# Kernel tuning notes

Hardware: AMD Instinct MI355X
Metric: run time of the kernel (lower is better)

The kernel has to match this reference:

```python
import jax, jax.numpy as jnp
import numpy as np

B, L, C, N, TN = 1, 256, 128, 4, 4
CH = N * C  # 512, flattened hidden for routing projections
EPS = 1.1920929e-07  # torch.finfo(float32).eps (RMSNorm default eps)
LN_EPS = 1e-5
N_SINKHORN = 20  # training-mode iteration count


def sinkhorn_knopp(raw, n_iters):
    # raw: [..., n, n] real-valued logits -> doubly-stochastic matrix
    M = jnp.exp(raw)
    for _ in range(n_iters):
        M = M / jnp.sum(M, axis=-1, keepdims=True)  # row normalize
        M = M / jnp.sum(M, axis=-2, keepdims=True)  # col normalize
    return M


def setup_inputs() -> dict:
    key = jax.random.key(0)
    ks = jax.random.split(key, 8)
    s = 0.02
    eye = jnp.eye(N, dtype=jnp.float32)
    b_res = 2.0 * eye + (-2.0) * (1.0 - eye)
    return {
        "p": jax.random.normal(ks[0], (B, L, L, C), jnp.float32),
        "p_mask": jnp.ones((B, L, L), jnp.float32),
        "W_pre": jax.random.normal(ks[1], (N, CH), jnp.float32) * s,
        "W_post": jax.random.normal(ks[2], (N, CH), jnp.float32) * s,
        "W_res": jax.random.normal(ks[3], (N * N, CH), jnp.float32) * s,
        "b_pre": jnp.zeros((1, N), jnp.float32),
        "b_post": jnp.zeros((1, N), jnp.float32),
        "b_res": b_res,
        "alpha_pre": jnp.asarray(0.01, jnp.float32),
        "alpha_post": jnp.asarray(0.01, jnp.float32),
        "alpha_res": jnp.asarray(0.01, jnp.float32),
        "ln_g": jnp.ones((C,), jnp.float32),
        "ln_b": jnp.zeros((C,), jnp.float32),
        "W1": jax.random.normal(ks[4], (TN * C, C), jnp.float32) * s,
        "b1": jnp.zeros((TN * C,), jnp.float32),
        "W2": jax.random.normal(ks[5], (C, TN * C), jnp.float32) * s,
        "b2": jnp.zeros((C,), jnp.float32),
    }


def reference(p, p_mask, W_pre, W_post, W_res, b_pre, b_post, b_res,
              alpha_pre, alpha_post, alpha_res, ln_g, ln_b, W1, b1, W2, b2):
    # expand_input: [B,L,L,C] -> [B,L,L,n,C]
    x = jnp.broadcast_to(p[..., None, :], (B, L, L, N, C))
    # --- compute_mappings ---
    xf = x.reshape(B, L, L, CH)
    xn = xf * jax.lax.rsqrt(jnp.mean(xf * xf, axis=-1, keepdims=True) + EPS)
    H_pre_dyn = jnp.tanh(xn @ W_pre.T)                      # [B,L,L,n]
    H_post_dyn = jnp.tanh(xn @ W_post.T)                    # [B,L,L,n]
    H_res_dyn = jnp.tanh(xn @ W_res.T).reshape(B, L, L, N, N)
    H_pre = jax.nn.sigmoid(alpha_pre * H_pre_dyn + b_pre)   # [B,L,L,n]
    H_post = 2.0 * jax.nn.sigmoid(alpha_post * H_post_dyn + b_post)
    H_res = sinkhorn_knopp(alpha_res * H_res_dyn + b_res, N_SINKHORN)  # [B,L,L,n,n]
    # contract: H_pre [B,L,L,1,n] @ x [B,L,L,n,C] -> [B,L,L,C]
    p_c = jnp.einsum('blkn,blknc->blkc', H_pre, x)
    # --- PairTransition (LN -> Linear -> ReLU -> Linear, masked) ---
    mu = jnp.mean(p_c, axis=-1, keepdims=True)
    var = jnp.mean(jnp.square(p_c - mu), axis=-1, keepdims=True)
    m = (p_c - mu) * jax.lax.rsqrt(var + LN_EPS) * ln_g + ln_b
    h = jax.nn.relu(m @ W1.T + b1)                          # [B,L,L,TN*C]
    p_t = (h @ W2.T + b2) * p_mask[..., None]
    p_updated = p_c + p_t
    # expand back: H_post^T [B,L,L,n,1] * p_updated [B,L,L,1,C]
    p_expanded = H_post[..., :, None] * p_updated[..., None, :]
    # residual mixing: [B,L,L,n,n] @ [B,L,L,n,C]
    p_residual = jnp.einsum('blkmn,blknc->blkmc', H_res, x)
    return p_residual + p_expanded  # [B,L,L,n,C]
```

## Files before the change

### kernel.cpp

```cpp
#include <hip/hip_runtime.h>
#include <stdint.h>

#define LLTOT 65536
#define CDIM  128
#define TPIX  32

typedef float f32x4  __attribute__((ext_vector_type(4)));
typedef float f32x16 __attribute__((ext_vector_type(16)));
typedef short s16x8  __attribute__((ext_vector_type(8)));

#define MFMA16(a, b, c) __builtin_amdgcn_mfma_f32_16x16x32_bf16((a), (b), (c), 0, 0, 0)
#define MFMA32(a, b, c) __builtin_amdgcn_mfma_f32_32x32x16_bf16((a), (b), (c), 0, 0, 0)

__device__ __align__(16) unsigned short g_wefff[2 * 4 * 64 * 8];
__device__ __align__(16) unsigned short g_w1gf[32 * 4 * 64 * 8];
__device__ __align__(16) unsigned short g_w2f [4 * 32 * 64 * 8];
__device__ __align__(16) float  g_hA[512];
__device__ __align__(16) float  g_w1gs[512];

__device__ __forceinline__ unsigned short f2bf(float f) {
    union { float f; uint32_t u; } v; v.f = f;
    uint32_t u = v.u;
    return (unsigned short)((u + 0x7FFFu + ((u >> 16) & 1u)) >> 16);
}
__device__ __forceinline__ uint32_t pack2(float a, float b) {
    uint32_t r;
    asm("v_cvt_pk_bf16_f32 %0, %1, %2" : "=v"(r) : "v"(a), "v"(b));
    return r;
}
__device__ __forceinline__ float bf2f(uint32_t lo16) { return __uint_as_float(lo16 << 16); }

__device__ __forceinline__ float fast_tanh(float x) {
    float cx = fminf(fmaxf(x, -10.f), 10.f);
    float e = __expf(2.f * cx);
    return (e - 1.f) * __builtin_amdgcn_rcpf(e + 1.f);
}
__device__ __forceinline__ float fast_sig(float z) {
    return __builtin_amdgcn_rcpf(1.f + __expf(-z));
}

__global__ void prep_kernel(const float* __restrict__ Wpre, const float* __restrict__ Wpost,
                            const float* __restrict__ Wres, const float* __restrict__ W1,
                            const float* __restrict__ W2, const float* __restrict__ ln_g,
                            const float* __restrict__ ln_b, const float* __restrict__ b1) {
    int b = blockIdx.x, t = threadIdx.x;
    if (b == 264) {
        int j = t;
        float sg = 0.f, sb = 0.f;
        const float* row = W1 + j * 128;
        #pragma unroll 4
        for (int c = 0; c < 128; c += 4) {
            float4 wv = *(const float4*)(row + c);
            float4 gv = *(const float4*)(ln_g + c);
            float4 bv = *(const float4*)(ln_b + c);
            sg += wv.x*gv.x + wv.y*gv.y + wv.z*gv.z + wv.w*gv.w;
            sb += wv.x*bv.x + wv.y*bv.y + wv.z*bv.z + wv.w*bv.w;
        }
        g_hA[j]   = b1[j] + sb;
        g_w1gs[j] = sg;
        return;
    }
    int idx = b * 512 + t;
    if (idx < 4096) {
        int e = idx & 7, lane = (idx >> 3) & 63, kk = (idx >> 9) & 3, tile = idx >> 11;
        int o = tile * 16 + (lane & 15);
        int c = kk * 32 + (lane >> 4) * 8 + e;
        float v = 0.f;
        if (o < 4)        v = Wpre[o*512+c] + Wpre[o*512+128+c] + Wpre[o*512+256+c] + Wpre[o*512+384+c];
        else if (o < 8)   { int j = o - 4;  v = Wpost[j*512+c] + Wpost[j*512+128+c] + Wpost[j*512+256+c] + Wpost[j*512+384+c]; }
        else if (o < 24)  { int j = o - 8;  v = Wres[j*512+c] + Wres[j*512+128+c] + Wres[j*512+256+c] + Wres[j*512+384+c]; }
        g_wefff[idx] = f2bf(v);
    } else if (idx < 69632) {
        int d = idx - 4096;
        int e = d & 7, lane = (d >> 3) & 63, kk = (d >> 9) & 3, jt = d >> 11;
        int j = jt * 16 + (lane & 15);
        int c = kk * 32 + (lane >> 4) * 8 + e;
        g_w1gf[d] = f2bf(W1[j * 128 + c] * ln_g[c]);
    } else if (idx < 135168) {
        int d = idx - 69632;
        int e = d & 7, lane = (d >> 3) & 63, kk = (d >> 9) & 31, ct = (d >> 14) & 3;
        int c = ct * 32 + (lane & 31);
        int k = kk * 16 + (lane >> 5) * 8 + e;
        g_w2f[d] = f2bf(W2[c * 512 + k]);
    }
}

__global__ void __launch_bounds__(512, 2) fused_kernel(
    const float* __restrict__ p, const float* __restrict__ p_mask,
    const float* __restrict__ b_pre, const float* __restrict__ b_post, const float* __restrict__ b_res,
    const float* __restrict__ a_pre, const float* __restrict__ a_post, const float* __restrict__ a_res,
    const float* __restrict__ b2g, float* __restrict__ out)
{
    __shared__ __align__(16) unsigned short pf_lds[8 * 64 * 8];
    __shared__ __align__(16) unsigned short h32[32 * 64 * 8];
    __shared__ __align__(16) float red_s[4096];
    __shared__ __align__(16) float A_s[128], B_s[128];
    __shared__ __align__(16) float2 simi_s[32];

    const int t = threadIdx.x;
    const int w = t >> 6, l = t & 63, lr = l & 15, lk = l >> 4;
    const size_t base = (size_t)blockIdx.x * TPIX;

    float M0 = 0.f, M1 = 0.f, M2 = 0.f, M3 = 0.f, sp = 0.f, hpm = 0.f;
    int mrow = 0, pix = 0;

    if (w < 2) {
        const int g = lk, pixl = lr;
        const size_t gpix = base + w * 16 + pixl;
        float apre = a_pre[0], apost = a_post[0], ares = a_res[0];
        float msk = p_mask[gpix];
        float bp0 = b_pre[0], bp1 = b_pre[1], bp2 = b_pre[2], bp3 = b_pre[3];
        float bq0 = b_post[0], bq1 = b_post[1], bq2 = b_post[2], bq3 = b_post[3];
        mrow = (g + 2) & 3;
        float br0 = b_res[mrow*4+0], br1 = b_res[mrow*4+1], br2 = b_res[mrow*4+2], br3 = b_res[mrow*4+3];

        float s = 0.f, ss = 0.f;
        s16x8 pf[4];
        const float* prow = p + gpix * 128 + g * 8;
        #pragma unroll
        for (int kk = 0; kk < 4; ++kk) {
            float4 va = *(const float4*)(prow + kk * 32);
            float4 vb = *(const float4*)(prow + kk * 32 + 4);
            s  += va.x + va.y + va.z + va.w + vb.x + vb.y + vb.z + vb.w;
            ss += va.x*va.x + va.y*va.y + va.z*va.z + va.w*va.w
                + vb.x*vb.x + vb.y*vb.y + vb.z*vb.z + vb.w*vb.w;
            union { s16x8 v; uint32_t u[4]; } cc;
            cc.u[0] = pack2(va.x, va.y);
            cc.u[1] = pack2(va.z, va.w);
            cc.u[2] = pack2(vb.x, vb.y);
            cc.u[3] = pack2(vb.z, vb.w);
            pf[kk] = cc.v;
            *(s16x8*)(pf_lds + (size_t)(w * 4 + kk) * 512 + l * 8) = cc.v;
        }
        s  += __shfl_xor(s, 16);  ss += __shfl_xor(ss, 16);
        s  += __shfl_xor(s, 32);  ss += __shfl_xor(ss, 32);
        float mu = s * (1.f / 128.f), mq = ss * (1.f / 128.f);
        float rv  = rsqrtf(mq + 1.1920929e-07f);
        float var = mq - mu * mu;

        f32x4 y1 = {0.f, 0.f, 0.f, 0.f}, y2 = {0.f, 0.f, 0.f, 0.f};
        #pragma unroll
        for (int kk = 0; kk < 4; ++kk) {
            s16x8 a0 = *(const s16x8*)(g_wefff + ((size_t)(kk) * 64 + l) * 8);
            s16x8 a1 = *(const s16x8*)(g_wefff + ((size_t)(4 + kk) * 64 + l) * 8);
            y1 = MFMA16(a0, pf[kk], y1);
            y2 = MFMA16(a1, pf[kk], y2);
        }
        #pragma unroll
        for (int r = 0; r < 4; ++r) { y1[r] *= rv; y2[r] *= rv; }

        float sp_loc = fast_sig(apre * fast_tanh(y1[0]) + bp0)
                     + fast_sig(apre * fast_tanh(y1[1]) + bp1)
                     + fast_sig(apre * fast_tanh(y1[2]) + bp2)
                     + fast_sig(apre * fast_tanh(y1[3]) + bp3);
        sp = __shfl(sp_loc, pixl);

        float hp0 = 2.f * fast_sig(apost * fast_tanh(y1[0]) + bq0);
        float hp1 = 2.f * fast_sig(apost * fast_tanh(y1[1]) + bq1);
        float hp2 = 2.f * fast_sig(apost * fast_tanh(y1[2]) + bq2);
        float hp3 = 2.f * fast_sig(apost * fast_tanh(y1[3]) + bq3);

        bool lo = g < 2;
        M0 = __expf(ares * fast_tanh(lo ? y2[0] : y1[0]) + br0);
        M1 = __expf(ares * fast_tanh(lo ? y2[1] : y1[1]) + br1);
        M2 = __expf(ares * fast_tanh(lo ? y2[2] : y1[2]) + br2);
        M3 = __expf(ares * fast_tanh(lo ? y2[3] : y1[3]) + br3);

        float h0b = __shfl(hp0, pixl + 16);
        float h1b = __shfl(hp1, pixl + 16);
        float h2b = __shfl(hp2, pixl + 16);
        float h3b = __shfl(hp3, pixl + 16);
        hpm = (mrow & 2) ? ((mrow & 1) ? h3b : h2b) : ((mrow & 1) ? h1b : h0b);

        pix = w * 16 + pixl;
        B_s[pix * 4 + mrow] = hpm * msk;
        if (l < 16) {
            float istd = rsqrtf(sp * sp * var + 1e-5f);
            simi_s[pix] = make_float2(sp * istd, sp * mu * istd);
        }
    }
    __syncthreads();

    if (w < 2) {
        #pragma unroll 1
        for (int it = 0; it < 20; ++it) {
            float ri = __builtin_amdgcn_rcpf(M0 + M1 + M2 + M3);
            M0 *= ri; M1 *= ri; M2 *= ri; M3 *= ri;
            float c0 = M0, c1 = M1, c2 = M2, c3 = M3;
            c0 += __shfl_xor(c0, 16); c1 += __shfl_xor(c1, 16); c2 += __shfl_xor(c2, 16); c3 += __shfl_xor(c3, 16);
            c0 += __shfl_xor(c0, 32); c1 += __shfl_xor(c1, 32); c2 += __shfl_xor(c2, 32); c3 += __shfl_xor(c3, 32);
            M0 *= __builtin_amdgcn_rcpf(c0); M1 *= __builtin_amdgcn_rcpf(c1);
            M2 *= __builtin_amdgcn_rcpf(c2); M3 *= __builtin_amdgcn_rcpf(c3);
        }
        float rm = M0 + M1 + M2 + M3;
        A_s[pix * 4 + mrow] = rm + hpm * sp;
    }

    s16x8 pfr[2][4];
    #pragma unroll
    for (int it = 0; it < 2; ++it)
        #pragma unroll
        for (int kk = 0; kk < 4; ++kk)
            pfr[it][kk] = *(const s16x8*)(pf_lds + (size_t)(it * 4 + kk) * 512 + l * 8);

    f32x4 acc1[4][2] = {};
    #pragma unroll
    for (int kk = 0; kk < 4; ++kk)
        #pragma unroll
        for (int jt = 0; jt < 4; ++jt) {
            s16x8 a = *(const s16x8*)(g_w1gf + ((size_t)((w * 4 + jt) * 4 + kk) * 64 + l) * 8);
            acc1[jt][0] = MFMA16(a, pfr[0][kk], acc1[jt][0]);
            acc1[jt][1] = MFMA16(a, pfr[1][kk], acc1[jt][1]);
        }

    {
        float2 sim0 = simi_s[lr];
        float2 sim1 = simi_s[16 + lr];
        #pragma unroll
        for (int jt = 0; jt < 4; ++jt) {
            int j0 = w * 64 + jt * 16 + lk * 4;
            float4 wg = *(const float4*)(g_w1gs + j0);
            float4 ha = *(const float4*)(g_hA + j0);
            #pragma unroll
            for (int it = 0; it < 2; ++it) {
                float si = it ? sim1.x : sim0.x;
                float mi = it ? sim1.y : sim0.y;
                f32x4 v = acc1[jt][it];
                float h0 = fmaxf(fmaf(si, v[0], fmaf(-mi, wg.x, ha.x)), 0.f);
                float h1 = fmaxf(fmaf(si, v[1], fmaf(-mi, wg.y, ha.y)), 0.f);
                float h2 = fmaxf(fmaf(si, v[2], fmaf(-mi, wg.z, ha.z)), 0.f);
                float h3 = fmaxf(fmaf(si, v[3], fmaf(-mi, wg.w, ha.w)), 0.f);
                uint2 uu;
                uu.x = pack2(h0, h1);
                uu.y = pack2(h2, h3);
                uint32_t addr = (uint32_t)((w * 4 + jt) * 1024
                              + (it * 16 + lr + 32 * (lk >> 1)) * 16 + (lk & 1) * 8);
                *(uint2*)((char*)h32 + addr) = uu;
            }
        }
    }
    __syncthreads();

    const int ct = w & 3, kh = w >> 2;
    f32x16 acc2 = {0.f,0.f,0.f,0.f, 0.f,0.f,0.f,0.f, 0.f,0.f,0.f,0.f, 0.f,0.f,0.f,0.f};
    #pragma unroll 4
    for (int kk2 = 0; kk2 < 16; ++kk2) {
        int ks = kh * 16 + kk2;
        s16x8 a = *(const s16x8*)(g_w2f + ((size_t)(ct * 32 + ks) * 64 + l) * 8);
        s16x8 b = *(const s16x8*)(h32 + (size_t)ks * 512 + l * 8);
        acc2 = MFMA32(a, b, acc2);
    }
    if (kh) {
        #pragma unroll
        for (int q = 0; q < 4; ++q) {
            f32x4 v = {acc2[4*q+0], acc2[4*q+1], acc2[4*q+2], acc2[4*q+3]};
            *(f32x4*)(red_s + ct * 1024 + q * 256 + l * 4) = v;
        }
    }
    __syncthreads();

    if (w < 4) {
        int i = l & 31;
        f32x4 Av = *(const f32x4*)(A_s + i * 4);
        f32x4 Bv = *(const f32x4*)(B_s + i * 4);
        #pragma unroll
        for (int q = 0; q < 4; ++q) {
            f32x4 r4 = *(const f32x4*)(red_s + ct * 1024 + q * 256 + l * 4);
            int cb = ct * 32 + 8 * q + 4 * (l >> 5);
            float4 b2v = *(const float4*)(b2g + cb);
            float d0 = acc2[4*q+0] + r4[0] + b2v.x;
            float d1 = acc2[4*q+1] + r4[1] + b2v.y;
            float d2 = acc2[4*q+2] + r4[2] + b2v.z;
            float d3 = acc2[4*q+3] + r4[3] + b2v.w;
            const unsigned short* pe = pf_lds
                + (size_t)(((l >> 4) & 1) * 4 + ct) * 512
                + ((l & 15) + 16 * q) * 8 + (l >> 5) * 4;
            uint2 pb = *(const uint2*)pe;
            float p0 = bf2f(pb.x & 0xffffu), p1 = __uint_as_float(pb.x & 0xffff0000u);
            float p2 = bf2f(pb.y & 0xffffu), p3 = __uint_as_float(pb.y & 0xffff0000u);
            float* og = out + (base + i) * 512 + cb;
            #pragma unroll
            for (int m = 0; m < 4; ++m) {
                f32x4 o;
                o[0] = Av[m] * p0 + Bv[m] * d0;
                o[1] = Av[m] * p1 + Bv[m] * d1;
                o[2] = Av[m] * p2 + Bv[m] * d2;
                o[3] = Av[m] * p3 + Bv[m] * d3;
                *(f32x4*)(og + m * 128) = o;
            }
        }
    }
}

extern "C" void kernel_launch(void* const* d_in, const int* in_sizes, int n_in,
                              void* d_out, int out_size, void* d_ws, size_t ws_size,
                              hipStream_t stream) {
    const float* p      = (const float*)d_in[0];
    const float* p_mask = (const float*)d_in[1];
    const float* W_pre  = (const float*)d_in[2];
    const float* W_post = (const float*)d_in[3];
    const float* W_res  = (const float*)d_in[4];
    const float* b_pre  = (const float*)d_in[5];
    const float* b_post = (const float*)d_in[6];
    const float* b_res  = (const float*)d_in[7];
    const float* a_pre  = (const float*)d_in[8];
    const float* a_post = (const float*)d_in[9];
    const float* a_res  = (const float*)d_in[10];
    const float* ln_g   = (const float*)d_in[11];
    const float* ln_b   = (const float*)d_in[12];
    const float* W1     = (const float*)d_in[13];
    const float* b1     = (const float*)d_in[14];
    const float* W2     = (const float*)d_in[15];
    const float* b2     = (const float*)d_in[16];
    float* out = (float*)d_out;

    prep_kernel<<<265, 512, 0, stream>>>(W_pre, W_post, W_res, W1, W2, ln_g, ln_b, b1);
    fused_kernel<<<2048, 512, 0, stream>>>(p, p_mask, b_pre, b_post, b_res,
                                           a_pre, a_post, a_res, b2, out);
}
```

Before: 87.09 us.

## Make each wave process its own 16 pixels end-to-end without block barriers

Restructures the fused kernel so each wavefront owns 16 pixels and runs routing, Sinkhorn, both MLP GEMMs and the output itself. The hidden layer is produced in 128-wide chunks staged through per-wave double-buffered LDS, and W2 is re-laid out for 16x16 MFMA. This removes the __syncthreads barriers, the idle waves during the routing and Sinkhorn phases, and the cross-wave split-K reduction through shared memory. In exchange, every wave now streams all of W1 and W2 from global/L2 for only 16 pixels, so weight traffic per pixel doubles, and accumulator register pressure rises.

Result: slower. 129.6 us (+48.9%).

```diff
diff --git a/kernel.cpp b/kernel.cpp
--- a/kernel.cpp
+++ b/kernel.cpp
@@ -3,18 +3,17 @@
 
 #define LLTOT 65536
 #define CDIM  128
-#define TPIX  32
-
-typedef float f32x4  __attribute__((ext_vector_type(4)));
-typedef float f32x16 __attribute__((ext_vector_type(16)));
-typedef short s16x8  __attribute__((ext_vector_type(8)));
+#define WPB   4
+#define NBLK  (LLTOT / (WPB * 16))
+
+typedef float f32x4 __attribute__((ext_vector_type(4)));
+typedef short s16x8 __attribute__((ext_vector_type(8)));
 
 #define MFMA16(a, b, c) __builtin_amdgcn_mfma_f32_16x16x32_bf16((a), (b), (c), 0, 0, 0)
-#define MFMA32(a, b, c) __builtin_amdgcn_mfma_f32_32x32x16_bf16((a), (b), (c), 0, 0, 0)
 
 __device__ __align__(16) unsigned short g_wefff[2 * 4 * 64 * 8];
 __device__ __align__(16) unsigned short g_w1gf[32 * 4 * 64 * 8];
-__device__ __align__(16) unsigned short g_w2f [4 * 32 * 64 * 8];
+__device__ __align__(16) unsigned short g_w2f16[16 * 8 * 64 * 8];
 __device__ __align__(16) float  g_hA[512];
 __device__ __align__(16) float  g_w1gs[512];
 
@@ -78,44 +77,41 @@
         g_w1gf[d] = f2bf(W1[j * 128 + c] * ln_g[c]);
     } else if (idx < 135168) {
         int d = idx - 69632;
-        int e = d & 7, lane = (d >> 3) & 63, kk = (d >> 9) & 31, ct = (d >> 14) & 3;
-        int c = ct * 32 + (lane & 31);
-        int k = kk * 16 + (lane >> 5) * 8 + e;
-        g_w2f[d] = f2bf(W2[c * 512 + k]);
-    }
-}
-
-__global__ void __launch_bounds__(512, 2) fused_kernel(
+        int e = d & 7, lane = (d >> 3) & 63, ct = (d >> 9) & 7, ksg = d >> 12;
+        int c = ct * 16 + (lane & 15);
+        int k = ksg * 32 + (lane >> 4) * 8 + e;
+        g_w2f16[d] = f2bf(W2[c * 512 + k]);
+    }
+}
+
+__global__ void fused_kernel(
     const float* __restrict__ p, const float* __restrict__ p_mask,
     const float* __restrict__ b_pre, const float* __restrict__ b_post, const float* __restrict__ b_res,
     const float* __restrict__ a_pre, const float* __restrict__ a_post, const float* __restrict__ a_res,
     const float* __restrict__ b2g, float* __restrict__ out)
 {
-    __shared__ __align__(16) unsigned short pf_lds[8 * 64 * 8];
-    __shared__ __align__(16) unsigned short h32[32 * 64 * 8];
-    __shared__ __align__(16) float red_s[4096];
-    __shared__ __align__(16) float A_s[128], B_s[128];
-    __shared__ __align__(16) float2 simi_s[32];
+    __shared__ __align__(16) unsigned short pf_lds[WPB][4 * 512];
+    __shared__ __align__(16) unsigned short h_lds[WPB][2][4 * 512];
 
     const int t = threadIdx.x;
     const int w = t >> 6, l = t & 63, lr = l & 15, lk = l >> 4;
-    const size_t base = (size_t)blockIdx.x * TPIX;
-
-    float M0 = 0.f, M1 = 0.f, M2 = 0.f, M3 = 0.f, sp = 0.f, hpm = 0.f;
-    int mrow = 0, pix = 0;
-
-    if (w < 2) {
+    const size_t gbase = ((size_t)blockIdx.x * WPB + w) * 16;
+
+    unsigned short* pfb = pf_lds[w];
+
+    float Aval, Bval, si, mi;
+    s16x8 pf[4];
+    {
         const int g = lk, pixl = lr;
-        const size_t gpix = base + w * 16 + pixl;
+        const size_t gpix = gbase + pixl;
         float apre = a_pre[0], apost = a_post[0], ares = a_res[0];
         float msk = p_mask[gpix];
         float bp0 = b_pre[0], bp1 = b_pre[1], bp2 = b_pre[2], bp3 = b_pre[3];
         float bq0 = b_post[0], bq1 = b_post[1], bq2 = b_post[2], bq3 = b_post[3];
-        mrow = (g + 2) & 3;
+        int mrow = (g + 2) & 3;
         float br0 = b_res[mrow*4+0], br1 = b_res[mrow*4+1], br2 = b_res[mrow*4+2], br3 = b_res[mrow*4+3];
 
         float s = 0.f, ss = 0.f;
-        s16x8 pf[4];
         const float* prow = p + gpix * 128 + g * 8;
         #pragma unroll
         for (int kk = 0; kk < 4; ++kk) {
@@ -130,7 +126,7 @@
             cc.u[2] = pack2(vb.x, vb.y);
             cc.u[3] = pack2(vb.z, vb.w);
             pf[kk] = cc.v;
-            *(s16x8*)(pf_lds + (size_t)(w * 4 + kk) * 512 + l * 8) = cc.v;
+            *(s16x8*)(pfb + kk * 512 + l * 8) = cc.v;
         }
         s  += __shfl_xor(s, 16);  ss += __shfl_xor(ss, 16);
         s  += __shfl_xor(s, 32);  ss += __shfl_xor(ss, 32);
@@ -153,7 +149,7 @@
                      + fast_sig(apre * fast_tanh(y1[1]) + bp1)
                      + fast_sig(apre * fast_tanh(y1[2]) + bp2)
                      + fast_sig(apre * fast_tanh(y1[3]) + bp3);
-        sp = __shfl(sp_loc, pixl);
+        float sp = __shfl(sp_loc, pixl);
 
         float hp0 = 2.f * fast_sig(apost * fast_tanh(y1[0]) + bq0);
         float hp1 = 2.f * fast_sig(apost * fast_tanh(y1[1]) + bq1);
@@ -161,27 +157,10 @@
         float hp3 = 2.f * fast_sig(apost * fast_tanh(y1[3]) + bq3);
 
         bool lo = g < 2;
-        M0 = __expf(ares * fast_tanh(lo ? y2[0] : y1[0]) + br0);
-        M1 = __expf(ares * fast_tanh(lo ? y2[1] : y1[1]) + br1);
-        M2 = __expf(ares * fast_tanh(lo ? y2[2] : y1[2]) + br2);
-        M3 = __expf(ares * fast_tanh(lo ? y2[3] : y1[3]) + br3);
-
-        float h0b = __shfl(hp0, pixl + 16);
-        float h1b = __shfl(hp1, pixl + 16);
-        float h2b = __shfl(hp2, pixl + 16);
-        float h3b = __shfl(hp3, pixl + 16);
-        hpm = (mrow & 2) ? ((mrow & 1) ? h3b : h2b) : ((mrow & 1) ? h1b : h0b);
-
-        pix = w * 16 + pixl;
-        B_s[pix * 4 + mrow] = hpm * msk;
-        if (l < 16) {
-            float istd = rsqrtf(sp * sp * var + 1e-5f);
-            simi_s[pix] = make_float2(sp * istd, sp * mu * istd);
-        }
-    }
-    __syncthreads();
-
-    if (w < 2) {
+        float M0 = __expf(ares * fast_tanh(lo ? y2[0] : y1[0]) + br0);
+        float M1 = __expf(ares * fast_tanh(lo ? y2[1] : y1[1]) + br1);
+        float M2 = __expf(ares * fast_tanh(lo ? y2[2] : y1[2]) + br2);
+        float M3 = __expf(ares * fast_tanh(lo ? y2[3] : y1[3]) + br3);
         #pragma unroll 1
         for (int it = 0; it < 20; ++it) {
             float ri = __builtin_amdgcn_rcpf(M0 + M1 + M2 + M3);
@@ -193,101 +172,94 @@
             M2 *= __builtin_amdgcn_rcpf(c2); M3 *= __builtin_amdgcn_rcpf(c3);
         }
         float rm = M0 + M1 + M2 + M3;
-        A_s[pix * 4 + mrow] = rm + hpm * sp;
-    }
-
-    s16x8 pfr[2][4];
-    #pragma unroll
-    for (int it = 0; it < 2; ++it)
+
+        float h0b = __shfl(hp0, pixl + 16);
+        float h1b = __shfl(hp1, pixl + 16);
+        float h2b = __shfl(hp2, pixl + 16);
+        float h3b = __shfl(hp3, pixl + 16);
+        float hpm = (mrow & 2) ? ((mrow & 1) ? h3b : h2b) : ((mrow & 1) ? h1b : h0b);
+
+        Aval = rm + hpm * sp;
+        Bval = hpm * msk;
+        float istd = rsqrtf(sp * sp * var + 1e-5f);
+        si = sp * istd;
+        mi = sp * mu * istd;
+    }
+
+    f32x4 acc2[8] = {};
+    #pragma unroll 1
+    for (int chunk = 0; chunk < 4; ++chunk) {
+        unsigned short* hb = h_lds[w][chunk & 1];
+
+        f32x4 acc1[8] = {};
         #pragma unroll
         for (int kk = 0; kk < 4; ++kk)
-            pfr[it][kk] = *(const s16x8*)(pf_lds + (size_t)(it * 4 + kk) * 512 + l * 8);
-
-    f32x4 acc1[4][2] = {};
-    #pragma unroll
-    for (int kk = 0; kk < 4; ++kk)
-        #pragma unroll
-        for (int jt = 0; jt < 4; ++jt) {
-            s16x8 a = *(const s16x8*)(g_w1gf + ((size_t)((w * 4 + jt) * 4 + kk) * 64 + l) * 8);
-            acc1[jt][0] = MFMA16(a, pfr[0][kk], acc1[jt][0]);
-            acc1[jt][1] = MFMA16(a, pfr[1][kk], acc1[jt][1]);
-        }
-
-    {
-        float2 sim0 = simi_s[lr];
-        float2 sim1 = simi_s[16 + lr];
-        #pragma unroll
-        for (int jt = 0; jt < 4; ++jt) {
-            int j0 = w * 64 + jt * 16 + lk * 4;
+            #pragma unroll
+            for (int jt = 0; jt < 8; ++jt) {
+                s16x8 a = *(const s16x8*)(g_w1gf + ((size_t)((chunk * 8 + jt) * 4 + kk) * 64 + l) * 8);
+                acc1[jt] = MFMA16(a, pf[kk], acc1[jt]);
+            }
+
+        #pragma unroll
+        for (int jt = 0; jt < 8; ++jt) {
+            int j0 = chunk * 128 + jt * 16 + lk * 4;
             float4 wg = *(const float4*)(g_w1gs + j0);
             float4 ha = *(const float4*)(g_hA + j0);
+            f32x4 v = acc1[jt];
+            float h0 = fmaxf(fmaf(si, v[0], fmaf(-mi, wg.x, ha.x)), 0.f);
+            float h1 = fmaxf(fmaf(si, v[1], fmaf(-mi, wg.y, ha.y)), 0.f);
+            float h2 = fmaxf(fmaf(si, v[2], fmaf(-mi, wg.z, ha.z)), 0.f);
+            float h3 = fmaxf(fmaf(si, v[3], fmaf(-mi, wg.w, ha.w)), 0.f);
+            uint2 uu;
+            uu.x = pack2(h0, h1);
+            uu.y = pack2(h2, h3);
+            int addr_sh = (jt >> 1) * 512 + (lr + 16 * ((jt & 1) * 2 + (lk >> 1))) * 8 + (lk & 1) * 4;
+            *(uint2*)(hb + addr_sh) = uu;
+        }
+
+        asm volatile("s_waitcnt lgkmcnt(0)" ::: "memory");
+        __builtin_amdgcn_sched_barrier(0);
+
+        #pragma unroll
+        for (int ks = 0; ks < 4; ++ks) {
+            s16x8 b = *(const s16x8*)(hb + ks * 512 + l * 8);
             #pragma unroll
-            for (int it = 0; it < 2; ++it) {
-                float si = it ? sim1.x : sim0.x;
-                float mi = it ? sim1.y : sim0.y;
-                f32x4 v = acc1[jt][it];
-                float h0 = fmaxf(fmaf(si, v[0], fmaf(-mi, wg.x, ha.x)), 0.f);
-                float h1 = fmaxf(fmaf(si, v[1], fmaf(-mi, wg.y, ha.y)), 0.f);
-                float h2 = fmaxf(fmaf(si, v[2], fmaf(-mi, wg.z, ha.z)), 0.f);
-                float h3 = fmaxf(fmaf(si, v[3], fmaf(-mi, wg.w, ha.w)), 0.f);
-                uint2 uu;
-                uu.x = pack2(h0, h1);
-                uu.y = pack2(h2, h3);
-                uint32_t addr = (uint32_t)((w * 4 + jt) * 1024
-                              + (it * 16 + lr + 32 * (lk >> 1)) * 16 + (lk & 1) * 8);
-                *(uint2*)((char*)h32 + addr) = uu;
+            for (int ct = 0; ct < 8; ++ct) {
+                s16x8 a = *(const s16x8*)(g_w2f16 + ((size_t)((chunk * 4 + ks) * 8 + ct) * 64 + l) * 8);
+                acc2[ct] = MFMA16(a, b, acc2[ct]);
             }
         }
     }
-    __syncthreads();
-
-    const int ct = w & 3, kh = w >> 2;
-    f32x16 acc2 = {0.f,0.f,0.f,0.f, 0.f,0.f,0.f,0.f, 0.f,0.f,0.f,0.f, 0.f,0.f,0.f,0.f};
-    #pragma unroll 4
-    for (int kk2 = 0; kk2 < 16; ++kk2) {
-        int ks = kh * 16 + kk2;
-        s16x8 a = *(const s16x8*)(g_w2f + ((size_t)(ct * 32 + ks) * 64 + l) * 8);
-        s16x8 b = *(const s16x8*)(h32 + (size_t)ks * 512 + l * 8);
-        acc2 = MFMA32(a, b, acc2);
-    }
-    if (kh) {
-        #pragma unroll
-        for (int q = 0; q < 4; ++q) {
-            f32x4 v = {acc2[4*q+0], acc2[4*q+1], acc2[4*q+2], acc2[4*q+3]};
-            *(f32x4*)(red_s + ct * 1024 + q * 256 + l * 4) = v;
-        }
-    }
-    __syncthreads();
-
-    if (w < 4) {
-        int i = l & 31;
-        f32x4 Av = *(const f32x4*)(A_s + i * 4);
-        f32x4 Bv = *(const f32x4*)(B_s + i * 4);
-        #pragma unroll
-        for (int q = 0; q < 4; ++q) {
-            f32x4 r4 = *(const f32x4*)(red_s + ct * 1024 + q * 256 + l * 4);
-            int cb = ct * 32 + 8 * q + 4 * (l >> 5);
-            float4 b2v = *(const float4*)(b2g + cb);
-            float d0 = acc2[4*q+0] + r4[0] + b2v.x;
-            float d1 = acc2[4*q+1] + r4[1] + b2v.y;
-            float d2 = acc2[4*q+2] + r4[2] + b2v.z;
-            float d3 = acc2[4*q+3] + r4[3] + b2v.w;
-            const unsigned short* pe = pf_lds
-                + (size_t)(((l >> 4) & 1) * 4 + ct) * 512
-                + ((l & 15) + 16 * q) * 8 + (l >> 5) * 4;
-            uint2 pb = *(const uint2*)pe;
-            float p0 = bf2f(pb.x & 0xffffu), p1 = __uint_as_float(pb.x & 0xffff0000u);
-            float p2 = bf2f(pb.y & 0xffffu), p3 = __uint_as_float(pb.y & 0xffff0000u);
-            float* og = out + (base + i) * 512 + cb;
-            #pragma unroll
-            for (int m = 0; m < 4; ++m) {
-                f32x4 o;
-                o[0] = Av[m] * p0 + Bv[m] * d0;
-                o[1] = Av[m] * p1 + Bv[m] * d1;
-                o[2] = Av[m] * p2 + Bv[m] * d2;
-                o[3] = Av[m] * p3 + Bv[m] * d3;
-                *(f32x4*)(og + m * 128) = o;
-            }
+
+    float Am[4], Bm[4];
+    #pragma unroll
+    for (int m = 0; m < 4; ++m) {
+        int src = lr + 16 * ((m + 2) & 3);
+        Am[m] = __shfl(Aval, src);
+        Bm[m] = __shfl(Bval, src);
+    }
+    float* og0 = out + (gbase + lr) * 512 + lk * 4;
+    #pragma unroll
+    for (int ct = 0; ct < 8; ++ct) {
+        float4 b2v = *(const float4*)(b2g + ct * 16 + lk * 4);
+        const unsigned short* pe = pfb + (ct >> 1) * 512
+            + (lr + 16 * ((2 * ct + (lk >> 1)) & 3)) * 8 + (lk & 1) * 4;
+        uint2 pb = *(const uint2*)pe;
+        float p0 = bf2f(pb.x & 0xffffu), p1 = __uint_as_float(pb.x & 0xffff0000u);
+        float p2 = bf2f(pb.y & 0xffffu), p3 = __uint_as_float(pb.y & 0xffff0000u);
+        float d0 = acc2[ct][0] + b2v.x;
+        float d1 = acc2[ct][1] + b2v.y;
+        float d2 = acc2[ct][2] + b2v.z;
+        float d3 = acc2[ct][3] + b2v.w;
+        float* og = og0 + ct * 16;
+        #pragma unroll
+        for (int m = 0; m < 4; ++m) {
+            f32x4 o;
+            o[0] = Am[m] * p0 + Bm[m] * d0;
+            o[1] = Am[m] * p1 + Bm[m] * d1;
+            o[2] = Am[m] * p2 + Bm[m] * d2;
+            o[3] = Am[m] * p3 + Bm[m] * d3;
+            *(f32x4*)(og + m * 128) = o;
         }
     }
 }
@@ -315,6 +287,6 @@
     float* out = (float*)d_out;
 
     prep_kernel<<<265, 512, 0, stream>>>(W_pre, W_post, W_res, W1, W2, ln_g, ln_b, b1);
-    fused_kernel<<<2048, 512, 0, stream>>>(p, p_mask, b_pre, b_post, b_res,
-                                           a_pre, a_post, a_res, b2, out);
-}
+    fused_kernel<<<NBLK, WPB * 64, 0, stream>>>(p, p_mask, b_pre, b_post, b_res,
+                                                a_pre, a_post, a_res, b2, out);
+}
```
